# Performance work log

Hardware: AMD Instinct MI355X
Metric: run time of the kernel (lower is better)

## Reference

```python
import jax, jax.numpy as jnp
import numpy as np

N_NODES = 20000
N_EDGES = 320000
NFEAT = 50
ALPHA = 0.2  # leaky relu slope
EPS = 1e-16


def _gat_head(x, src, dst, W, a, concat):
    # x: (N, Fin), W: (Fin, Fout), a: (2*Fout,)
    N = x.shape[0]
    Wh = x @ W                      # (N, Fout)
    Fout = W.shape[1]
    # edge_h @ a == Wh[src] @ a[:Fout] + Wh[dst] @ a[Fout:]
    s_src = Wh @ a[:Fout]           # (N,)
    s_dst = Wh @ a[Fout:]           # (N,)
    e = jax.nn.leaky_relu(s_src[src] + s_dst[dst], negative_slope=ALPHA)  # (E,)
    # segment softmax over incoming edges of each target node
    e_max = jax.ops.segment_max(e, dst, num_segments=N)   # (N,)
    e_exp = jnp.exp(e - e_max[dst])                         # (E,)
    e_sum = jax.ops.segment_sum(e_exp, dst, num_segments=N)
    att = e_exp / (e_sum[dst] + EPS)                        # (E,)
    msg = Wh[src] * att[:, None]                            # (E, Fout)
    h = jax.ops.segment_sum(msg, dst, num_segments=N)       # (N, Fout)
    return jax.nn.elu(h) if concat else h


def _multi_head(x, src, dst, W, a, concat):
    # W: (H, Fin, Fout), a: (H, 2*Fout) -> (H, N, Fout)
    return jax.vmap(_gat_head, in_axes=(None, None, None, 0, 0, None))(x, src, dst, W, a, concat)


def setup_inputs() -> dict:
    key = jax.random.key(0)
    ks = jax.random.split(key, 8)
    x = jax.random.normal(ks[0], (N_NODES, NFEAT), dtype=jnp.float32)
    edge_index = jax.random.randint(ks[1], (2, N_EDGES), 0, N_NODES, dtype=jnp.int64)
    s = 0.1
    W1 = jax.random.normal(ks[2], (4, NFEAT, 256), dtype=jnp.float32) * s
    a1 = jax.random.normal(ks[3], (4, 512), dtype=jnp.float32) * s
    W2 = jax.random.normal(ks[4], (4, 1024, 256), dtype=jnp.float32) * s
    a2 = jax.random.normal(ks[5], (4, 512), dtype=jnp.float32) * s
    W3 = jax.random.normal(ks[6], (6, 1024, 121), dtype=jnp.float32) * s
    a3 = jax.random.normal(ks[7], (6, 242), dtype=jnp.float32) * s
    return {"x": x, "edge_index": edge_index, "W1": W1, "a1": a1, "W2": W2, "a2": a2, "W3": W3, "a3": a3}


def reference(x, edge_index, W1, a1, W2, a2, W3, a3):
    src, dst = edge_index[0], edge_index[1]
    N = x.shape[0]
    # layer 1: 4 heads, concat -> (N, 1024), then elu
    h1 = _multi_head(x, src, dst, W1, a1, True)      # (4, N, 256)
    x1 = jnp.transpose(h1, (1, 0, 2)).reshape(N, -1)  # concat along feature dim
    x1 = jax.nn.elu(x1)
    # layer 2: 4 heads, concat + skip connection, then elu
    h2 = _multi_head(x1, src, dst, W2, a2, True)
    x2 = jnp.transpose(h2, (1, 0, 2)).reshape(N, -1)
    x2 = jax.nn.elu(x2 + x1)
    # layer 3: 6 heads, no concat-elu, mean over heads
    h3 = _multi_head(x2, src, dst, W3, a3, False)     # (6, N, 121)
    x3 = jnp.mean(h3, axis=0)
    return jax.nn.sigmoid(x3)
```

## Files before the change

kernel.cpp:

```cpp
#include <hip/hip_runtime.h>
#include <cstdint>

#define N_NODES 20000
#define N_EDGES 320000
#define ALPHA 0.2f
#define GAT_EPS 1e-16f
#define MPAD 20096
#define RBLK 157
#define RHI 20
#define SCAN_BLKS 80
#define BT_ROWS 1152

typedef __attribute__((ext_vector_type(8))) _Float16 half8;
typedef __attribute__((ext_vector_type(4))) _Float16 half4t;
typedef __attribute__((ext_vector_type(16))) float f32x16;
typedef __attribute__((ext_vector_type(2))) float f32x2;

__device__ __forceinline__ float elu1(float x) { return x > 0.f ? x : __expf(x) - 1.f; }

__device__ __forceinline__ unsigned char f2fp8(float x) {
    return (unsigned char)(__builtin_amdgcn_cvt_pk_fp8_f32(x, 0.f, 0, false) & 0xff);
}

__device__ __forceinline__ void async16(const void* g, void* l) {
    __builtin_amdgcn_global_load_lds(
        (const __attribute__((address_space(1))) unsigned int*)g,
        (__attribute__((address_space(3))) unsigned int*)l, 16, 0, 0);
}

__device__ __forceinline__ float rdlanef(float v, int j) {
    return __int_as_float(__builtin_amdgcn_readlane(__float_as_int(v), j));
}

__global__ void hist_kernel(const int* __restrict__ dst, int* __restrict__ counts, int E) {
    int e = blockIdx.x * blockDim.x + threadIdx.x;
    if (e < E) atomicAdd(&counts[dst[e]], 1);
}

__global__ void scan1_kernel(const int* __restrict__ counts, int* __restrict__ excl,
                             int* __restrict__ partial, int N) {
    __shared__ int sh[256];
    int t = threadIdx.x, b = blockIdx.x;
    int i = b * 256 + t;
    int v = (i < N) ? counts[i] : 0;
    sh[t] = v;
    __syncthreads();
    for (int d = 1; d < 256; d <<= 1) {
        int x = (t >= d) ? sh[t - d] : 0;
        __syncthreads();
        sh[t] += x;
        __syncthreads();
    }
    if (i < N) excl[i] = sh[t] - v;
    if (t == 255) partial[b] = sh[255];
}

__global__ void scan2_kernel(int* __restrict__ partial) {
    __shared__ int sh[128];
    int t = threadIdx.x;
    int v = (t < SCAN_BLKS) ? partial[t] : 0;
    sh[t] = v;
    __syncthreads();
    for (int d = 1; d < 128; d <<= 1) {
        int x = (t >= d) ? sh[t - d] : 0;
        __syncthreads();
        sh[t] += x;
        __syncthreads();
    }
    if (t < SCAN_BLKS) partial[t] = sh[t] - v;
}

__global__ void scan3_kernel(const int* __restrict__ excl, const int* __restrict__ partial,
                             int* __restrict__ rowptr, int* __restrict__ cursor, int N, int E) {
    int t = threadIdx.x, b = blockIdx.x;
    int i = b * 256 + t;
    if (i < N) {
        int v = excl[i] + partial[b];
        rowptr[i] = v;
        cursor[i] = v;
    }
    if (i == 0) rowptr[N] = E;
}

__global__ void scatter_kernel(const int* __restrict__ src, const int* __restrict__ dst,
                               int* __restrict__ cursor, int* __restrict__ esrc, int E) {
    int e = blockIdx.x * blockDim.x + threadIdx.x;
    if (e < E) {
        int p = atomicAdd(&cursor[dst[e]], 1);
        esrc[p] = src[e];
    }
}

__global__ void pack_x16(const float* __restrict__ x, _Float16* __restrict__ A) {
    int idx = blockIdx.x * 256 + threadIdx.x;
    int r = idx >> 6, c = idx & 63;
    float v = (r < N_NODES && c < 50) ? x[r * 50 + c] : 0.f;
    A[idx] = (_Float16)v;
}

__global__ void pack_bt1(const float* __restrict__ W, _Float16* __restrict__ Bt) {
    int idx = blockIdx.x * 256 + threadIdx.x;
    int c = idx >> 6, k = idx & 63;
    int h = c >> 8, f = c & 255;
    float v = (k < 50) ? W[((size_t)h * 50 + k) * 256 + f] : 0.f;
    Bt[idx] = (_Float16)v;
}

__global__ void pack_bt16(const float* __restrict__ W, _Float16* __restrict__ Bt,
                          int F, int Fpad, int Ctot) {
    int c = blockIdx.y;
    int k = blockIdx.x * blockDim.x + threadIdx.x;
    float v = 0.f;
    if (c < Ctot) {
        int h = c / Fpad, f = c - h * Fpad;
        if (f < F) v = W[(size_t)h * 1024 * F + (size_t)k * F + f];
    }
    Bt[(size_t)c * 1024 + k] = (_Float16)v;
}

__global__ __launch_bounds__(64) void wtilde_kernel(const float* __restrict__ W,
                                                    const float* __restrict__ a,
                                                    _Float16* __restrict__ BT, int Kreal,
                                                    int Kdim, int F, int H, int Nfeat) {
    int k = blockIdx.x, j = blockIdx.y;
    if (j >= 2 * H) return;
    int lane = threadIdx.x;
    int h = j < H ? j : j - H;
    int ao = j < H ? 0 : F;
    float s = 0.f;
    if (k < Kreal) {
        const float* wp = W + ((size_t)h * Kreal + k) * F;
        const float* ap = a + (size_t)h * 2 * F + ao;
        for (int f = lane; f < F; f += 64) s += wp[f] * ap[f];
    }
#pragma unroll
    for (int off = 32; off; off >>= 1) s += __shfl_down(s, off);
    if (lane == 0) BT[(size_t)(Nfeat + j) * Kdim + k] = (_Float16)s;
}

__global__ __launch_bounds__(256) void gemm_f16(const _Float16* __restrict__ A,
                                                const _Float16* __restrict__ BT,
                                                unsigned char* __restrict__ C8,
                                                float* __restrict__ SPRE,
                                                int M, int Nfeat, int ld, int Kdim, int Cblk,
                                                int ldA, int mode) {
    int id = blockIdx.x;
    int xm = id & 7, q = id >> 3;
    int cb = q % Cblk, rh = q / Cblk;
    int rb = rh * 8 + xm;
    if (rb >= RBLK) return;
    __shared__ __align__(16) _Float16 sA[128 * 64];
    __shared__ __align__(16) _Float16 sB[128 * 64];
    int t = threadIdx.x;
    int row0 = rb * 128, col0 = cb * 128;
    int lane = t & 63, wave = t >> 6;
    int wm = wave >> 1, wn = wave & 1;
    int l31 = lane & 31;
    int lhi = lane >> 5;

    int koff = (mode == 1) ? ((cb >> 1) * 64) : 0;
    const _Float16* gA = A + (size_t)row0 * ldA + koff;
    const _Float16* gB = BT + (size_t)col0 * Kdim;

    int sR[4], sgl[4];
#pragma unroll
    for (int i = 0; i < 4; i++) {
        int m = i * 256 + t;
        sR[i] = m >> 3;
        sgl[i] = (m & 7) ^ (sR[i] & 7);
    }

    f32x16 acc[2][2] = {};

    for (int k0 = 0; k0 < Kdim; k0 += 64) {
        __syncthreads();
#pragma unroll
        for (int i = 0; i < 4; i++) {
            const _Float16* pa = gA + (size_t)sR[i] * ldA + k0 + sgl[i] * 8;
            const _Float16* pb = gB + (size_t)sR[i] * Kdim + k0 + sgl[i] * 8;
            async16(pa, sA + (i * 256 + t) * 8);
            async16(pb, sB + (i * 256 + t) * 8);
        }
        __syncthreads();
#pragma unroll
        for (int kk = 0; kk < 4; kk++) {
            int g = kk * 2 + lhi;
            half8 af[2], bf[2];
#pragma unroll
            for (int mt = 0; mt < 2; mt++) {
                int R = wm * 64 + mt * 32 + l31;
                int gp = g ^ (R & 7);
                af[mt] = *(const half8*)(sA + R * 64 + gp * 8);
            }
#pragma unroll
            for (int nt = 0; nt < 2; nt++) {
                int R = wn * 64 + nt * 32 + l31;
                int gp = g ^ (R & 7);
                bf[nt] = *(const half8*)(sB + R * 64 + gp * 8);
            }
#pragma unroll
            for (int mt = 0; mt < 2; mt++)
#pragma unroll
                for (int nt = 0; nt < 2; nt++)
                    acc[mt][nt] = __builtin_amdgcn_mfma_f32_32x32x16_f16(af[mt], bf[nt], acc[mt][nt], 0, 0, 0);
        }
    }

    int cb32 = col0 + wn * 64 + l31;
    int rb32 = row0 + wm * 64 + 4 * lhi;
    if (mode == 1) {
        _Float16* C16 = (_Float16*)C8;
#pragma unroll
        for (int mt = 0; mt < 2; mt++)
#pragma unroll
            for (int nt = 0; nt < 2; nt++) {
                int gc = cb32 + nt * 32;
                if (gc < Nfeat) {
#pragma unroll
                    for (int r = 0; r < 16; r++) {
                        int gr = rb32 + mt * 32 + (r & 3) + 8 * (r >> 2);
                        if (gr < M) C16[(size_t)gr * ld + gc] = (_Float16)elu1(elu1(acc[mt][nt][r]));
                    }
                }
            }
        return;
    }
#pragma unroll
    for (int mt = 0; mt < 2; mt++)
#pragma unroll
        for (int nt = 0; nt < 2; nt++) {
            int gc = cb32 + nt * 32;
            if (gc < Nfeat) {
#pragma unroll
                for (int r = 0; r < 16; r++) {
                    int gr = rb32 + mt * 32 + (r & 3) + 8 * (r >> 2);
                    if (gr < M) C8[(size_t)gr * ld + gc] = f2fp8(acc[mt][nt][r]);
                }
            } else if (gc < Nfeat + 12) {
                int j = gc - Nfeat;
#pragma unroll
                for (int r = 0; r < 16; r++) {
                    int gr = rb32 + mt * 32 + (r & 3) + 8 * (r >> 2);
                    if (gr < M) SPRE[(size_t)j * N_NODES + gr] = acc[mt][nt][r];
                }
            }
        }
}

__global__ __launch_bounds__(256) void aggx1_kernel(const int* __restrict__ rowptr,
                                                    const int* __restrict__ esrc,
                                                    const float* __restrict__ SPRE,
                                                    const _Float16* __restrict__ A1,
                                                    _Float16* __restrict__ XB, int N) {
    int n = blockIdx.x;
    int h = threadIdx.x >> 6;
    int lane = threadIdx.x & 63;
    int start = rowptr[n], end = rowptr[n + 1];
    int cnt = end - start;
    const float* ss = SPRE + (size_t)h * N;
    float sd = SPRE[(size_t)(4 + h) * N + n];
    const unsigned char* Wb = (const unsigned char*)A1 + 2 * lane;
    float acc = 0.f;

    if (cnt <= 64) {
        int e = start + lane;
        bool act = e < end;
        int idx = act ? esrc[e] : 0;
        int voff = idx << 7;

        unsigned short wA[8], wB[8], wC[8], wD[8];
        auto ISSUE = [&](unsigned short (&buf)[8], int base) {
#pragma unroll
            for (int u = 0; u < 8; u++) {
                int off = __builtin_amdgcn_readlane(voff, base + u);
                buf[u] = *(const unsigned short*)(Wb + (unsigned)off);
            }
        };
        ISSUE(wA, 0);
        if (cnt > 8)  ISSUE(wB, 8);
        if (cnt > 16) ISSUE(wC, 16);
        if (cnt > 24) ISSUE(wD, 24);

        float sc = -1e30f;
        if (act) {
            sc = ss[idx] + sd;
            sc = sc > 0.f ? sc : ALPHA * sc;
        }
        float m = sc;
#pragma unroll
        for (int off = 1; off < 64; off <<= 1) m = fmaxf(m, __shfl_xor(m, off));
        float ptil = act ? __expf(sc - m) : 0.f;
        float s = ptil;
#pragma unroll
        for (int off = 1; off < 64; off <<= 1) s += __shfl_xor(s, off);
        float p = ptil * (1.f / (s + GAT_EPS));

        auto CONSUME = [&](unsigned short (&buf)[8], int base) {
#pragma unroll
            for (int u = 0; u < 8; u++) {
                float pj = rdlanef(p, base + u);
                acc += pj * (float)(*(const _Float16*)&buf[u]);
            }
        };
        CONSUME(wA, 0);
        if (cnt > 8)  { if (cnt > 32) ISSUE(wA, 32); CONSUME(wB, 8); }
        if (cnt > 16) { if (cnt > 40) ISSUE(wB, 40); CONSUME(wC, 16); }
        if (cnt > 24) { if (cnt > 48) ISSUE(wC, 48); CONSUME(wD, 24); }
        if (cnt > 32) { if (cnt > 56) ISSUE(wD, 56); CONSUME(wA, 32); }
        if (cnt > 40) CONSUME(wB, 40);
        if (cnt > 48) CONSUME(wC, 48);
        if (cnt > 56) CONSUME(wD, 56);
    } else {
        float m = -1e30f, s = 0.f;
        int sidx = 0; float ssc = -1e30f;
        for (int e0 = start; e0 < end; e0 += 64) {
            int e = e0 + lane;
            bool act = e < end;
            int idx = act ? esrc[e] : 0;
            float sc = -1e30f;
            if (act) {
                sc = ss[idx] + sd;
                sc = sc > 0.f ? sc : ALPHA * sc;
            }
            sidx = idx; ssc = sc;
            float mn = fmaxf(m, sc);
            s = s * __expf(m - mn) + (act ? __expf(sc - mn) : 0.f);
            m = mn;
        }
        float lm = m;
#pragma unroll
        for (int off = 1; off < 64; off <<= 1) m = fmaxf(m, __shfl_xor(m, off));
        float ptil = s * __expf(lm - m);
        s = ptil;
#pragma unroll
        for (int off = 1; off < 64; off <<= 1) s += __shfl_xor(s, off);
        float inv = 1.f / (s + GAT_EPS);

        int lastStart = start + (((end - start - 1) >> 6) << 6);
        for (int e0 = start; e0 < end; e0 += 64) {
            int e = e0 + lane;
            bool act = e < end;
            int idx; float p;
            if (e0 == lastStart) {
                idx = sidx;
                p = act ? __expf(ssc - m) * inv : 0.f;
            } else {
                idx = act ? esrc[e] : 0;
                float sc = -1e30f;
                if (act) {
                    sc = ss[idx] + sd;
                    sc = sc > 0.f ? sc : ALPHA * sc;
                }
                p = act ? __expf(sc - m) * inv : 0.f;
            }
            int cn = end - e0; if (cn > 64) cn = 64;
            for (int j = 0; j < cn; j++) {
                int ij = __builtin_amdgcn_readlane(idx, j);
                float pj = rdlanef(p, j);
                unsigned short w = *(const unsigned short*)(Wb + ((size_t)(unsigned)ij << 7));
                acc += pj * (float)(*(const _Float16*)&w);
            }
        }
    }

    XB[(size_t)n * 256 + h * 64 + lane] = (_Float16)acc;
}

__global__ __launch_bounds__(256) void attagg256_kernel(const int* __restrict__ rowptr,
                                                        const int* __restrict__ esrc,
                                                        const float* __restrict__ SPRE,
                                                        const unsigned char* __restrict__ WH8,
                                                        _Float16* __restrict__ X16,
                                                        int use_skip, int N) {
    int n = blockIdx.x;
    int h = threadIdx.x >> 6;
    int lane = threadIdx.x & 63;
    int start = rowptr[n], end = rowptr[n + 1];
    int cnt = end - start;
    const float* ss = SPRE + (size_t)h * N;
    float sd = SPRE[(size_t)(4 + h) * N + n];
    const unsigned char* Wb = WH8 + h * 256 + lane * 4;
    float a0 = 0.f, a1 = 0.f, a2 = 0.f, a3 = 0.f;

    if (cnt <= 64) {
        int e = start + lane;
        bool act = e < end;
        int idx = act ? esrc[e] : 0;

        unsigned int wA[8], wB[8], wC[8], wD[8];
        auto ISSUE = [&](unsigned int (&buf)[8], int base) {
#pragma unroll
            for (int u = 0; u < 8; u++) {
                int ij = __builtin_amdgcn_readlane(idx, base + u);
                buf[u] = *(const unsigned int*)(Wb + ((size_t)(unsigned)ij << 10));
            }
        };
        ISSUE(wA, 0);
        if (cnt > 8)  ISSUE(wB, 8);
        if (cnt > 16) ISSUE(wC, 16);
        if (cnt > 24) ISSUE(wD, 24);

        float sc = -1e30f;
        if (act) {
            sc = ss[idx] + sd;
            sc = sc > 0.f ? sc : ALPHA * sc;
        }
        float m = sc;
#pragma unroll
        for (int off = 1; off < 64; off <<= 1) m = fmaxf(m, __shfl_xor(m, off));
        float ptil = act ? __expf(sc - m) : 0.f;
        float s = ptil;
#pragma unroll
        for (int off = 1; off < 64; off <<= 1) s += __shfl_xor(s, off);
        float p = ptil * (1.f / (s + GAT_EPS));

        auto CONSUME = [&](unsigned int (&buf)[8], int base) {
#pragma unroll
            for (int u = 0; u < 8; u++) {
                float pj = rdlanef(p, base + u);
                f32x2 lo = __builtin_amdgcn_cvt_pk_f32_fp8((int)buf[u], false);
                f32x2 hi = __builtin_amdgcn_cvt_pk_f32_fp8((int)buf[u], true);
                a0 += pj * lo.x; a1 += pj * lo.y; a2 += pj * hi.x; a3 += pj * hi.y;
            }
        };
        CONSUME(wA, 0);
        if (cnt > 8)  { if (cnt > 32) ISSUE(wA, 32); CONSUME(wB, 8); }
        if (cnt > 16) { if (cnt > 40) ISSUE(wB, 40); CONSUME(wC, 16); }
        if (cnt > 24) { if (cnt > 48) ISSUE(wC, 48); CONSUME(wD, 24); }
        if (cnt > 32) { if (cnt > 56) ISSUE(wD, 56); CONSUME(wA, 32); }
        if (cnt > 40) CONSUME(wB, 40);
        if (cnt > 48) CONSUME(wC, 48);
        if (cnt > 56) CONSUME(wD, 56);
    } else {
        float m = -1e30f, s = 0.f;
        int sidx = 0; float ssc = -1e30f;
        for (int e0 = start; e0 < end; e0 += 64) {
            int e = e0 + lane;
            bool act = e < end;
            int idx = act ? esrc[e] : 0;
            float sc = -1e30f;
            if (act) {
                sc = ss[idx] + sd;
                sc = sc > 0.f ? sc : ALPHA * sc;
            }
            sidx = idx; ssc = sc;
            float mn = fmaxf(m, sc);
            s = s * __expf(m - mn) + (act ? __expf(sc - mn) : 0.f);
            m = mn;
        }
        float lm = m;
#pragma unroll
        for (int off = 1; off < 64; off <<= 1) m = fmaxf(m, __shfl_xor(m, off));
        float ptil = s * __expf(lm - m);
        s = ptil;
#pragma unroll
        for (int off = 1; off < 64; off <<= 1) s += __shfl_xor(s, off);
        float inv = 1.f / (s + GAT_EPS);

        int lastStart = start + (((end - start - 1) >> 6) << 6);
        for (int e0 = start; e0 < end; e0 += 64) {
            int e = e0 + lane;
            bool act = e < end;
            int idx; float p;
            if (e0 == lastStart) {
                idx = sidx;
                p = act ? __expf(ssc - m) * inv : 0.f;
            } else {
                idx = act ? esrc[e] : 0;
                float sc = -1e30f;
                if (act) {
                    sc = ss[idx] + sd;
                    sc = sc > 0.f ? sc : ALPHA * sc;
                }
                p = act ? __expf(sc - m) * inv : 0.f;
            }
            int cn = end - e0; if (cn > 64) cn = 64;
            for (int j = 0; j < cn; j++) {
                int ij = __builtin_amdgcn_readlane(idx, j);
                float pj = rdlanef(p, j);
                unsigned int w = *(const unsigned int*)(Wb + (size_t)ij * 1024);
                f32x2 lo = __builtin_amdgcn_cvt_pk_f32_fp8((int)w, false);
                f32x2 hi = __builtin_amdgcn_cvt_pk_f32_fp8((int)w, true);
                a0 += pj * lo.x; a1 += pj * lo.y; a2 += pj * hi.x; a3 += pj * hi.y;
            }
        }
    }

    size_t o = (size_t)n * 1024 + h * 256 + lane * 4;
    float v0, v1, v2, v3;
    if (use_skip) {
        half4t sk = *(const half4t*)(X16 + o);
        v0 = elu1(elu1(a0) + (float)sk.x);
        v1 = elu1(elu1(a1) + (float)sk.y);
        v2 = elu1(elu1(a2) + (float)sk.z);
        v3 = elu1(elu1(a3) + (float)sk.w);
    } else {
        v0 = elu1(elu1(a0)); v1 = elu1(elu1(a1));
        v2 = elu1(elu1(a2)); v3 = elu1(elu1(a3));
    }
    half4t r;
    r.x = (_Float16)v0; r.y = (_Float16)v1; r.z = (_Float16)v2; r.w = (_Float16)v3;
    *(half4t*)(X16 + o) = r;
}

__global__ __launch_bounds__(384) void attagg726_kernel(const int* __restrict__ rowptr,
                                                        const int* __restrict__ esrc,
                                                        const float* __restrict__ SPRE,
                                                        const unsigned char* __restrict__ WH8,
                                                        float* __restrict__ out, int N) {
    __shared__ float part[6][124];
    int n = blockIdx.x;
    int t = threadIdx.x;
    int h = t >> 6;
    int lane = t & 63;
    int start = rowptr[n], end = rowptr[n + 1];
    int cnt = end - start;
    const float* ss = SPRE + (size_t)h * N;
    float sd = SPRE[(size_t)(6 + h) * N + n];
    const unsigned char* Wb = WH8 + h * 124 + 2 * lane;
    float a0 = 0.f, a1 = 0.f;

    if (cnt <= 64) {
        int e = start + lane;
        bool act = e < end;
        int idx = act ? esrc[e] : 0;

        unsigned short wA[8], wB[8], wC[8], wD[8];
        auto ISSUE = [&](unsigned short (&buf)[8], int base) {
#pragma unroll
            for (int u = 0; u < 8; u++) {
                int ij = __builtin_amdgcn_readlane(idx, base + u);
                buf[u] = *(const unsigned short*)(Wb + (size_t)(unsigned)ij * 768u);
            }
        };
        ISSUE(wA, 0);
        if (cnt > 8)  ISSUE(wB, 8);
        if (cnt > 16) ISSUE(wC, 16);
        if (cnt > 24) ISSUE(wD, 24);

        float sc = -1e30f;
        if (act) {
            sc = ss[idx] + sd;
            sc = sc > 0.f ? sc : ALPHA * sc;
        }
        float m = sc;
#pragma unroll
        for (int off = 1; off < 64; off <<= 1) m = fmaxf(m, __shfl_xor(m, off));
        float ptil = act ? __expf(sc - m) : 0.f;
        float s = ptil;
#pragma unroll
        for (int off = 1; off < 64; off <<= 1) s += __shfl_xor(s, off);
        float p = ptil * (1.f / (s + GAT_EPS));

        auto CONSUME = [&](unsigned short (&buf)[8], int base) {
#pragma unroll
            for (int u = 0; u < 8; u++) {
                float pj = rdlanef(p, base + u);
                f32x2 f = __builtin_amdgcn_cvt_pk_f32_fp8((int)buf[u], false);
                a0 += pj * f.x; a1 += pj * f.y;
            }
        };
        CONSUME(wA, 0);
        if (cnt > 8)  { if (cnt > 32) ISSUE(wA, 32); CONSUME(wB, 8); }
        if (cnt > 16) { if (cnt > 40) ISSUE(wB, 40); CONSUME(wC, 16); }
        if (cnt > 24) { if (cnt > 48) ISSUE(wC, 48); CONSUME(wD, 24); }
        if (cnt > 32) { if (cnt > 56) ISSUE(wD, 56); CONSUME(wA, 32); }
        if (cnt > 40) CONSUME(wB, 40);
        if (cnt > 48) CONSUME(wC, 48);
        if (cnt > 56) CONSUME(wD, 56);
    } else {
        float m = -1e30f, s = 0.f;
        int sidx = 0; float ssc = -1e30f;
        for (int e0 = start; e0 < end; e0 += 64) {
            int e = e0 + lane;
            bool act = e < end;
            int idx = act ? esrc[e] : 0;
            float sc = -1e30f;
            if (act) {
                sc = ss[idx] + sd;
                sc = sc > 0.f ? sc : ALPHA * sc;
            }
            sidx = idx; ssc = sc;
            float mn = fmaxf(m, sc);
            s = s * __expf(m - mn) + (act ? __expf(sc - mn) : 0.f);
            m = mn;
        }
        float lm = m;
#pragma unroll
        for (int off = 1; off < 64; off <<= 1) m = fmaxf(m, __shfl_xor(m, off));
        float ptil = s * __expf(lm - m);
        s = ptil;
#pragma unroll
        for (int off = 1; off < 64; off <<= 1) s += __shfl_xor(s, off);
        float inv = 1.f / (s + GAT_EPS);

        int lastStart = start + (((end - start - 1) >> 6) << 6);
        for (int e0 = start; e0 < end; e0 += 64) {
            int e = e0 + lane;
            bool act = e < end;
            int idx; float p;
            if (e0 == lastStart) {
                idx = sidx;
                p = act ? __expf(ssc - m) * inv : 0.f;
            } else {
                idx = act ? esrc[e] : 0;
                float sc = -1e30f;
                if (act) {
                    sc = ss[idx] + sd;
                    sc = sc > 0.f ? sc : ALPHA * sc;
                }
                p = act ? __expf(sc - m) * inv : 0.f;
            }
            int cn = end - e0; if (cn > 64) cn = 64;
            for (int j = 0; j < cn; j++) {
                int ij = __builtin_amdgcn_readlane(idx, j);
                float pj = rdlanef(p, j);
                unsigned short w = *(const unsigned short*)(Wb + (size_t)ij * 768);
                f32x2 f = __builtin_amdgcn_cvt_pk_f32_fp8((int)w, false);
                a0 += pj * f.x; a1 += pj * f.y;
            }
        }
    }

    if (lane < 62) {
        part[h][2 * lane]     = a0;
        part[h][2 * lane + 1] = a1;
    }
    __syncthreads();
    if (t < 121) {
        float tot = (part[0][t] + part[1][t] + part[2][t] +
                     part[3][t] + part[4][t] + part[5][t]) * (1.f / 6.f);
        out[(size_t)n * 121 + t] = 1.f / (1.f + __expf(-tot));
    }
}

extern "C" void kernel_launch(void* const* d_in, const int* in_sizes, int n_in,
                              void* d_out, int out_size, void* d_ws, size_t ws_size,
                              hipStream_t stream) {
    const float* x  = (const float*)d_in[0];
    const int*   ei = (const int*)d_in[1];
    const float* W1 = (const float*)d_in[2];
    const float* a1 = (const float*)d_in[3];
    const float* W2 = (const float*)d_in[4];
    const float* a2 = (const float*)d_in[5];
    const float* W3 = (const float*)d_in[6];
    const float* a3 = (const float*)d_in[7];
    float* out = (float*)d_out;
    const int N = N_NODES, E = N_EDGES;
    const int* src = ei;
    const int* dst = ei + E;

    char* ws = (char*)d_ws;
    size_t off = 0;
    auto alloc = [&](size_t b) { size_t o = off; off += (b + 255) & ~(size_t)255; return o; };
    _Float16* X16  = (_Float16*)(ws + alloc((size_t)MPAD * 1024 * 2));
    unsigned char* WH8 = (unsigned char*)(ws + alloc((size_t)MPAD * 1024));
    _Float16* BT16 = (_Float16*)(ws + alloc((size_t)BT_ROWS * 1024 * 2));
    _Float16* A1   = (_Float16*)(ws + alloc((size_t)MPAD * 64 * 2));
    _Float16* BT1  = (_Float16*)(ws + alloc((size_t)BT_ROWS * 64 * 2));
    _Float16* XB   = (_Float16*)(ws + alloc((size_t)MPAD * 256 * 2));
    _Float16* BTS  = (_Float16*)(ws + alloc((size_t)128 * 64 * 2));
    float* SPRE   = (float*)(ws + alloc((size_t)12 * N * 4));
    int*   rowptr = (int*)(ws + alloc((size_t)(N + 1) * 4));
    int*   cursor = (int*)(ws + alloc((size_t)N * 4));
    int*   counts = (int*)(ws + alloc((size_t)N * 4));
    int*   excl   = (int*)(ws + alloc((size_t)N * 4));
    int*   partial= (int*)(ws + alloc((size_t)SCAN_BLKS * 4));
    int*   esrc   = (int*)(ws + alloc((size_t)E * 4));

    hipMemsetAsync(counts, 0, (size_t)N * 4, stream);
    hist_kernel<<<(E + 255) / 256, 256, 0, stream>>>(dst, counts, E);
    scan1_kernel<<<SCAN_BLKS, 256, 0, stream>>>(counts, excl, partial, N);
    scan2_kernel<<<1, 128, 0, stream>>>(partial);
    scan3_kernel<<<SCAN_BLKS, 256, 0, stream>>>(excl, partial, rowptr, cursor, N, E);
    scatter_kernel<<<(E + 255) / 256, 256, 0, stream>>>(src, dst, cursor, esrc, E);
    hipMemsetAsync(X16 + (size_t)N * 1024, 0, (size_t)(MPAD - N) * 1024 * 2, stream);
    hipMemsetAsync(XB + (size_t)N * 256, 0, (size_t)(MPAD - N) * 256 * 2, stream);

    pack_x16<<<MPAD * 64 / 256, 256, 0, stream>>>(x, A1);
    pack_bt1<<<1024 * 64 / 256, 256, 0, stream>>>(W1, BT1);
    wtilde_kernel<<<dim3(64, 8), 64, 0, stream>>>(W1, a1, BTS, 50, 64, 256, 4, 0);
    gemm_f16<<<8 * RHI * 1, 256, 0, stream>>>(A1, BTS, WH8, SPRE, N, 0, 1024, 64, 1, 64, 0);
    aggx1_kernel<<<N, 256, 0, stream>>>(rowptr, esrc, SPRE, A1, XB, N);
    gemm_f16<<<8 * RHI * 8, 256, 0, stream>>>(XB, BT1, (unsigned char*)X16, SPRE, N, 1024, 1024, 64, 8, 256, 1);

    pack_bt16<<<dim3(4, 1024), 256, 0, stream>>>(W2, BT16, 256, 256, 1024);
    wtilde_kernel<<<dim3(1024, 8), 64, 0, stream>>>(W2, a2, BT16, 1024, 1024, 256, 4, 1024);
    gemm_f16<<<8 * RHI * 9, 256, 0, stream>>>(X16, BT16, WH8, SPRE, N, 1024, 1024, 1024, 9, 1024, 0);
    attagg256_kernel<<<N, 256, 0, stream>>>(rowptr, esrc, SPRE, WH8, X16, 1, N);

    pack_bt16<<<dim3(4, 744), 256, 0, stream>>>(W3, BT16, 121, 124, 744);
    wtilde_kernel<<<dim3(1024, 12), 64, 0, stream>>>(W3, a3, BT16, 1024, 1024, 121, 6, 744);
    gemm_f16<<<8 * RHI * 6, 256, 0, stream>>>(X16, BT16, WH8, SPRE, N, 744, 768, 1024, 6, 1024, 0);
    attagg726_kernel<<<N, 384, 0, stream>>>(rowptr, esrc, SPRE, WH8, out, N);
}
```

Baseline: 434.2 us.

## Split aggregation across edges per wave with 16-byte row loads and LDS reduction

The layer-2 and layer-3 aggregation kernels now give each wave a strided subset of edges instead of one head. Each lane loads 16 contiguous fp8 bytes of a full neighbor row and accumulates with packed FMA, and per-wave partials are summed through shared memory. To keep rows aligned, the layer-3 projection output is padded to 128 columns per head with a 1024-byte stride. The aim is wider, fully coalesced gathers with more loads in flight, at the cost of extra LDS traffic, two block barriers and a slightly larger layer-3 GEMM.

```diff
diff --git a/kernel.cpp b/kernel.cpp
--- a/kernel.cpp
+++ b/kernel.cpp
@@ -30,6 +30,17 @@
 
 __device__ __forceinline__ float rdlanef(float v, int j) {
     return __int_as_float(__builtin_amdgcn_readlane(__float_as_int(v), j));
+}
+
+__device__ __forceinline__ f32x2 pkfma(f32x2 a, f32x2 b, f32x2 c) {
+    f32x2 d;
+    asm("v_pk_fma_f32 %0, %1, %2, %3" : "=v"(d) : "v"(a), "v"(b), "v"(c));
+    return d;
+}
+
+template <bool HI>
+__device__ __forceinline__ f32x2 cvt8(unsigned int u) {
+    return __builtin_amdgcn_cvt_pk_f32_fp8((int)u, HI);
 }
 
 __global__ void hist_kernel(const int* __restrict__ dst, int* __restrict__ counts, int E) {
@@ -372,33 +383,33 @@
                                                         const unsigned char* __restrict__ WH8,
                                                         _Float16* __restrict__ X16,
                                                         int use_skip, int N) {
+    __shared__ float Pp[4][66];
+    __shared__ float part[4][1152];
     int n = blockIdx.x;
-    int h = threadIdx.x >> 6;
-    int lane = threadIdx.x & 63;
+    int t = threadIdx.x;
+    int wv = t >> 6;
+    int lane = t & 63;
     int start = rowptr[n], end = rowptr[n + 1];
     int cnt = end - start;
-    const float* ss = SPRE + (size_t)h * N;
-    float sd = SPRE[(size_t)(4 + h) * N + n];
-    const unsigned char* Wb = WH8 + h * 256 + lane * 4;
-    float a0 = 0.f, a1 = 0.f, a2 = 0.f, a3 = 0.f;
+    const float* ss = SPRE + (size_t)wv * N;
+    float sd = SPRE[(size_t)(4 + wv) * N + n];
 
     if (cnt <= 64) {
         int e = start + lane;
         bool act = e < end;
         int idx = act ? esrc[e] : 0;
 
-        unsigned int wA[8], wB[8], wC[8], wD[8];
-        auto ISSUE = [&](unsigned int (&buf)[8], int base) {
-#pragma unroll
-            for (int u = 0; u < 8; u++) {
-                int ij = __builtin_amdgcn_readlane(idx, base + u);
-                buf[u] = *(const unsigned int*)(Wb + ((size_t)(unsigned)ij << 10));
-            }
-        };
-        ISSUE(wA, 0);
-        if (cnt > 8)  ISSUE(wB, 8);
-        if (cnt > 16) ISSUE(wC, 16);
-        if (cnt > 24) ISSUE(wD, 24);
+        const unsigned char* Wp = WH8 + lane * 16;
+        uint4 w = {}, wnext = {};
+        bool has0 = wv < cnt, has1 = wv + 4 < cnt;
+        if (has0) {
+            int i0 = __builtin_amdgcn_readlane(idx, wv);
+            w = *(const uint4*)(Wp + ((size_t)(unsigned)i0 << 10));
+        }
+        if (has1) {
+            int i1 = __builtin_amdgcn_readlane(idx, wv + 4);
+            wnext = *(const uint4*)(Wp + ((size_t)(unsigned)i1 << 10));
+        }
 
         float sc = -1e30f;
         if (act) {
@@ -413,25 +424,42 @@
 #pragma unroll
         for (int off = 1; off < 64; off <<= 1) s += __shfl_xor(s, off);
         float p = ptil * (1.f / (s + GAT_EPS));
-
-        auto CONSUME = [&](unsigned int (&buf)[8], int base) {
-#pragma unroll
-            for (int u = 0; u < 8; u++) {
-                float pj = rdlanef(p, base + u);
-                f32x2 lo = __builtin_amdgcn_cvt_pk_f32_fp8((int)buf[u], false);
-                f32x2 hi = __builtin_amdgcn_cvt_pk_f32_fp8((int)buf[u], true);
-                a0 += pj * lo.x; a1 += pj * lo.y; a2 += pj * hi.x; a3 += pj * hi.y;
-            }
-        };
-        CONSUME(wA, 0);
-        if (cnt > 8)  { if (cnt > 32) ISSUE(wA, 32); CONSUME(wB, 8); }
-        if (cnt > 16) { if (cnt > 40) ISSUE(wB, 40); CONSUME(wC, 16); }
-        if (cnt > 24) { if (cnt > 48) ISSUE(wC, 48); CONSUME(wD, 24); }
-        if (cnt > 32) { if (cnt > 56) ISSUE(wD, 56); CONSUME(wA, 32); }
-        if (cnt > 40) CONSUME(wB, 40);
-        if (cnt > 48) CONSUME(wC, 48);
-        if (cnt > 56) CONSUME(wD, 56);
+        Pp[wv][lane] = p;
+        __syncthreads();
+
+        f32x2 acc[8] = {};
+        int hf = lane >> 4;
+        if (has0) {
+            int j = wv;
+            for (;;) {
+                uint4 w3 = w;
+                bool have3 = j + 8 < cnt;
+                if (have3) {
+                    int i3 = __builtin_amdgcn_readlane(idx, j + 8);
+                    w3 = *(const uint4*)(Wp + ((size_t)(unsigned)i3 << 10));
+                }
+                float pj = Pp[hf][j];
+                f32x2 pv; pv.x = pj; pv.y = pj;
+                acc[0] = pkfma(cvt8<false>(w.x), pv, acc[0]);
+                acc[1] = pkfma(cvt8<true>(w.x),  pv, acc[1]);
+                acc[2] = pkfma(cvt8<false>(w.y), pv, acc[2]);
+                acc[3] = pkfma(cvt8<true>(w.y),  pv, acc[3]);
+                acc[4] = pkfma(cvt8<false>(w.z), pv, acc[4]);
+                acc[5] = pkfma(cvt8<true>(w.z),  pv, acc[5]);
+                acc[6] = pkfma(cvt8<false>(w.w), pv, acc[6]);
+                acc[7] = pkfma(cvt8<true>(w.w),  pv, acc[7]);
+                j += 4;
+                if (j >= cnt) break;
+                w = wnext; wnext = w3;
+            }
+        }
+#pragma unroll
+        for (int k2 = 0; k2 < 8; k2++)
+            *(f32x2*)&part[wv][lane * 18 + 2 * k2] = acc[k2];
     } else {
+        for (int i = lane; i < 1152; i += 64) part[wv][i] = 0.f;
+        const unsigned char* Wb = WH8 + wv * 256 + lane * 4;
+        float a0 = 0.f, a1 = 0.f, a2 = 0.f, a3 = 0.f;
         float m = -1e30f, s = 0.f;
         int sidx = 0; float ssc = -1e30f;
         for (int e0 = start; e0 < end; e0 += 64) {
@@ -478,15 +506,28 @@
             for (int j = 0; j < cn; j++) {
                 int ij = __builtin_amdgcn_readlane(idx, j);
                 float pj = rdlanef(p, j);
-                unsigned int w = *(const unsigned int*)(Wb + (size_t)ij * 1024);
-                f32x2 lo = __builtin_amdgcn_cvt_pk_f32_fp8((int)w, false);
-                f32x2 hi = __builtin_amdgcn_cvt_pk_f32_fp8((int)w, true);
+                unsigned int ww = *(const unsigned int*)(Wb + (size_t)ij * 1024);
+                f32x2 lo = __builtin_amdgcn_cvt_pk_f32_fp8((int)ww, false);
+                f32x2 hi = __builtin_amdgcn_cvt_pk_f32_fp8((int)ww, true);
                 a0 += pj * lo.x; a1 += pj * lo.y; a2 += pj * hi.x; a3 += pj * hi.y;
             }
         }
-    }
-
-    size_t o = (size_t)n * 1024 + h * 256 + lane * 4;
+        int cb = wv * 256 + lane * 4;
+        int off0 = (cb >> 4) * 18 + (cb & 15);
+        part[wv][off0]     = a0;
+        part[wv][off0 + 1] = a1;
+        part[wv][off0 + 2] = a2;
+        part[wv][off0 + 3] = a3;
+    }
+    __syncthreads();
+
+    int off = (t >> 2) * 18 + 4 * (t & 3);
+    float a0 = part[0][off]     + part[1][off]     + part[2][off]     + part[3][off];
+    float a1 = part[0][off + 1] + part[1][off + 1] + part[2][off + 1] + part[3][off + 1];
+    float a2 = part[0][off + 2] + part[1][off + 2] + part[2][off + 2] + part[3][off + 2];
+    float a3 = part[0][off + 3] + part[1][off + 3] + part[2][off + 3] + part[3][off + 3];
+
+    size_t o = (size_t)n * 1024 + t * 4;
     float v0, v1, v2, v3;
     if (use_skip) {
         half4t sk = *(const half4t*)(X16 + o);
@@ -508,35 +549,36 @@
                                                         const float* __restrict__ SPRE,
                                                         const unsigned char* __restrict__ WH8,
                                                         float* __restrict__ out, int N) {
-    __shared__ float part[6][124];
+    __shared__ float Pp[6][66];
+    __shared__ float part[6][864];
+    __shared__ float red[768];
     int n = blockIdx.x;
     int t = threadIdx.x;
-    int h = t >> 6;
+    int wv = t >> 6;
     int lane = t & 63;
     int start = rowptr[n], end = rowptr[n + 1];
     int cnt = end - start;
-    const float* ss = SPRE + (size_t)h * N;
-    float sd = SPRE[(size_t)(6 + h) * N + n];
-    const unsigned char* Wb = WH8 + h * 124 + 2 * lane;
-    float a0 = 0.f, a1 = 0.f;
+    const float* ss = SPRE + (size_t)wv * N;
+    float sd = SPRE[(size_t)(6 + wv) * N + n];
 
     if (cnt <= 64) {
         int e = start + lane;
         bool act = e < end;
         int idx = act ? esrc[e] : 0;
 
-        unsigned short wA[8], wB[8], wC[8], wD[8];
-        auto ISSUE = [&](unsigned short (&buf)[8], int base) {
-#pragma unroll
-            for (int u = 0; u < 8; u++) {
-                int ij = __builtin_amdgcn_readlane(idx, base + u);
-                buf[u] = *(const unsigned short*)(Wb + (size_t)(unsigned)ij * 768u);
-            }
-        };
-        ISSUE(wA, 0);
-        if (cnt > 8)  ISSUE(wB, 8);
-        if (cnt > 16) ISSUE(wC, 16);
-        if (cnt > 24) ISSUE(wD, 24);
+        const unsigned char* Wp = WH8 + lane * 16;
+        uint4 w = {}, wnext = {};
+        bool has0 = wv < cnt, has1 = wv + 6 < cnt;
+        if (lane < 48) {
+            if (has0) {
+                int i0 = __builtin_amdgcn_readlane(idx, wv);
+                w = *(const uint4*)(Wp + ((size_t)(unsigned)i0 << 10));
+            }
+            if (has1) {
+                int i1 = __builtin_amdgcn_readlane(idx, wv + 6);
+                wnext = *(const uint4*)(Wp + ((size_t)(unsigned)i1 << 10));
+            }
+        }
 
         float sc = -1e30f;
         if (act) {
@@ -551,24 +593,44 @@
 #pragma unroll
         for (int off = 1; off < 64; off <<= 1) s += __shfl_xor(s, off);
         float p = ptil * (1.f / (s + GAT_EPS));
-
-        auto CONSUME = [&](unsigned short (&buf)[8], int base) {
-#pragma unroll
-            for (int u = 0; u < 8; u++) {
-                float pj = rdlanef(p, base + u);
-                f32x2 f = __builtin_amdgcn_cvt_pk_f32_fp8((int)buf[u], false);
-                a0 += pj * f.x; a1 += pj * f.y;
-            }
-        };
-        CONSUME(wA, 0);
-        if (cnt > 8)  { if (cnt > 32) ISSUE(wA, 32); CONSUME(wB, 8); }
-        if (cnt > 16) { if (cnt > 40) ISSUE(wB, 40); CONSUME(wC, 16); }
-        if (cnt > 24) { if (cnt > 48) ISSUE(wC, 48); CONSUME(wD, 24); }
-        if (cnt > 32) { if (cnt > 56) ISSUE(wD, 56); CONSUME(wA, 32); }
-        if (cnt > 40) CONSUME(wB, 40);
-        if (cnt > 48) CONSUME(wC, 48);
-        if (cnt > 56) CONSUME(wD, 56);
+        Pp[wv][lane] = p;
+        __syncthreads();
+
+        f32x2 acc[8] = {};
+        if (lane < 48 && has0) {
+            int hf = lane >> 3;
+            int j = wv;
+            for (;;) {
+                uint4 w3 = w;
+                bool have3 = j + 12 < cnt;
+                if (have3) {
+                    int i3 = __builtin_amdgcn_readlane(idx, j + 12);
+                    w3 = *(const uint4*)(Wp + ((size_t)(unsigned)i3 << 10));
+                }
+                float pj = Pp[hf][j];
+                f32x2 pv; pv.x = pj; pv.y = pj;
+                acc[0] = pkfma(cvt8<false>(w.x), pv, acc[0]);
+                acc[1] = pkfma(cvt8<true>(w.x),  pv, acc[1]);
+                acc[2] = pkfma(cvt8<false>(w.y), pv, acc[2]);
+                acc[3] = pkfma(cvt8<true>(w.y),  pv, acc[3]);
+                acc[4] = pkfma(cvt8<false>(w.z), pv, acc[4]);
+                acc[5] = pkfma(cvt8<true>(w.z),  pv, acc[5]);
+                acc[6] = pkfma(cvt8<false>(w.w), pv, acc[6]);
+                acc[7] = pkfma(cvt8<true>(w.w),  pv, acc[7]);
+                j += 6;
+                if (j >= cnt) break;
+                w = wnext; wnext = w3;
+            }
+        }
+        if (lane < 48) {
+#pragma unroll
+            for (int k2 = 0; k2 < 8; k2++)
+                *(f32x2*)&part[wv][lane * 18 + 2 * k2] = acc[k2];
+        }
     } else {
+        for (int i = lane; i < 864; i += 64) part[wv][i] = 0.f;
+        const unsigned char* Wb = WH8 + wv * 128 + 2 * lane;
+        float a0 = 0.f, a1 = 0.f;
         float m = -1e30f, s = 0.f;
         int sidx = 0; float ssc = -1e30f;
         for (int e0 = start; e0 < end; e0 += 64) {
@@ -615,21 +677,27 @@
             for (int j = 0; j < cn; j++) {
                 int ij = __builtin_amdgcn_readlane(idx, j);
                 float pj = rdlanef(p, j);
-                unsigned short w = *(const unsigned short*)(Wb + (size_t)ij * 768);
-                f32x2 f = __builtin_amdgcn_cvt_pk_f32_fp8((int)w, false);
+                unsigned short ww = *(const unsigned short*)(Wb + ((size_t)(unsigned)ij << 10));
+                f32x2 f = __builtin_amdgcn_cvt_pk_f32_fp8((int)ww, false);
                 a0 += pj * f.x; a1 += pj * f.y;
             }
         }
-    }
-
-    if (lane < 62) {
-        part[h][2 * lane]     = a0;
-        part[h][2 * lane + 1] = a1;
+        int c0 = wv * 128 + 2 * lane;
+        part[wv][(c0 >> 4) * 18 + (c0 & 15)] = a0;
+        int c1 = c0 + 1;
+        part[wv][(c1 >> 4) * 18 + (c1 & 15)] = a1;
+    }
+    __syncthreads();
+
+    for (int c = t; c < 768; c += 384) {
+        int off = (c >> 4) * 18 + (c & 15);
+        red[c] = part[0][off] + part[1][off] + part[2][off] +
+                 part[3][off] + part[4][off] + part[5][off];
     }
     __syncthreads();
     if (t < 121) {
-        float tot = (part[0][t] + part[1][t] + part[2][t] +
-                     part[3][t] + part[4][t] + part[5][t]) * (1.f / 6.f);
+        float tot = (red[t] + red[128 + t] + red[256 + t] +
+                     red[384 + t] + red[512 + t] + red[640 + t]) * (1.f / 6.f);
         out[(size_t)n * 121 + t] = 1.f / (1.f + __expf(-tot));
     }
 }
@@ -689,8 +757,8 @@
     gemm_f16<<<8 * RHI * 9, 256, 0, stream>>>(X16, BT16, WH8, SPRE, N, 1024, 1024, 1024, 9, 1024, 0);
     attagg256_kernel<<<N, 256, 0, stream>>>(rowptr, esrc, SPRE, WH8, X16, 1, N);
 
-    pack_bt16<<<dim3(4, 744), 256, 0, stream>>>(W3, BT16, 121, 124, 744);
-    wtilde_kernel<<<dim3(1024, 12), 64, 0, stream>>>(W3, a3, BT16, 1024, 1024, 121, 6, 744);
-    gemm_f16<<<8 * RHI * 6, 256, 0, stream>>>(X16, BT16, WH8, SPRE, N, 744, 768, 1024, 6, 1024, 0);
+    pack_bt16<<<dim3(4, 768), 256, 0, stream>>>(W3, BT16, 121, 128, 768);
+    wtilde_kernel<<<dim3(1024, 12), 64, 0, stream>>>(W3, a3, BT16, 1024, 1024, 121, 6, 768);
+    gemm_f16<<<8 * RHI * 7, 256, 0, stream>>>(X16, BT16, WH8, SPRE, N, 768, 1024, 1024, 7, 1024, 0);
     attagg726_kernel<<<N, 384, 0, stream>>>(rowptr, esrc, SPRE, WH8, out, N);
 }
```

After: 438.6 us. About the same (+1.0%).

## Split layer-2 attention into softmax precompute and column-chunked aggregation kernel

Applied to the files above, without the earlier changes.

The fused layer-2 attention+aggregation kernel is split in two. A new att_kernel computes normalized edge attention per head into a buffer. A new agg256c_kernel gives each block 4 nodes times one 128-column chunk, so a wave gathers 2 fp8 bytes per lane instead of 4. Column chunks are ordered so that blocks sharing a chunk run close together, which should improve cache locality of the neighbour-row gathers. The cost is an extra launch, an attention buffer write and read, and more gather instructions in total.

```diff
diff --git a/kernel.cpp b/kernel.cpp
--- a/kernel.cpp
+++ b/kernel.cpp
@@ -30,6 +30,11 @@
 
 __device__ __forceinline__ float rdlanef(float v, int j) {
     return __int_as_float(__builtin_amdgcn_readlane(__float_as_int(v), j));
+}
+
+template <bool HI>
+__device__ __forceinline__ f32x2 cvt8(unsigned int u) {
+    return __builtin_amdgcn_cvt_pk_f32_fp8((int)u, HI);
 }
 
 __global__ void hist_kernel(const int* __restrict__ dst, int* __restrict__ counts, int E) {
@@ -366,33 +371,101 @@
     XB[(size_t)n * 256 + h * 64 + lane] = (_Float16)acc;
 }
 
-__global__ __launch_bounds__(256) void attagg256_kernel(const int* __restrict__ rowptr,
-                                                        const int* __restrict__ esrc,
-                                                        const float* __restrict__ SPRE,
-                                                        const unsigned char* __restrict__ WH8,
-                                                        _Float16* __restrict__ X16,
-                                                        int use_skip, int N) {
+__global__ void att_kernel(const int* __restrict__ rowptr, const int* __restrict__ esrc,
+                           const float* __restrict__ SPRE, float* __restrict__ ATT,
+                           int N, int H) {
     int n = blockIdx.x;
     int h = threadIdx.x >> 6;
     int lane = threadIdx.x & 63;
+    if (h >= H) return;
     int start = rowptr[n], end = rowptr[n + 1];
     int cnt = end - start;
     const float* ss = SPRE + (size_t)h * N;
-    float sd = SPRE[(size_t)(4 + h) * N + n];
-    const unsigned char* Wb = WH8 + h * 256 + lane * 4;
-    float a0 = 0.f, a1 = 0.f, a2 = 0.f, a3 = 0.f;
+    float sd = SPRE[(size_t)(H + h) * N + n];
+    float* ap = ATT + (size_t)h * N_EDGES;
 
     if (cnt <= 64) {
         int e = start + lane;
         bool act = e < end;
         int idx = act ? esrc[e] : 0;
-
-        unsigned int wA[8], wB[8], wC[8], wD[8];
-        auto ISSUE = [&](unsigned int (&buf)[8], int base) {
+        float sc = -1e30f;
+        if (act) {
+            sc = ss[idx] + sd;
+            sc = sc > 0.f ? sc : ALPHA * sc;
+        }
+        float m = sc;
+#pragma unroll
+        for (int off = 1; off < 64; off <<= 1) m = fmaxf(m, __shfl_xor(m, off));
+        float ptil = act ? __expf(sc - m) : 0.f;
+        float s = ptil;
+#pragma unroll
+        for (int off = 1; off < 64; off <<= 1) s += __shfl_xor(s, off);
+        if (act) ap[e] = ptil * (1.f / (s + GAT_EPS));
+    } else {
+        float m = -1e30f, s = 0.f;
+        for (int e0 = start; e0 < end; e0 += 64) {
+            int e = e0 + lane;
+            bool act = e < end;
+            int idx = act ? esrc[e] : 0;
+            float sc = -1e30f;
+            if (act) {
+                sc = ss[idx] + sd;
+                sc = sc > 0.f ? sc : ALPHA * sc;
+            }
+            float mn = fmaxf(m, sc);
+            s = s * __expf(m - mn) + (act ? __expf(sc - mn) : 0.f);
+            m = mn;
+        }
+        float lm = m;
+#pragma unroll
+        for (int off = 1; off < 64; off <<= 1) m = fmaxf(m, __shfl_xor(m, off));
+        float ptil = s * __expf(lm - m);
+        s = ptil;
+#pragma unroll
+        for (int off = 1; off < 64; off <<= 1) s += __shfl_xor(s, off);
+        float inv = 1.f / (s + GAT_EPS);
+        for (int e0 = start; e0 < end; e0 += 64) {
+            int e = e0 + lane;
+            if (e < end) {
+                int idx = esrc[e];
+                float sc = ss[idx] + sd;
+                sc = sc > 0.f ? sc : ALPHA * sc;
+                ap[e] = __expf(sc - m) * inv;
+            }
+        }
+    }
+}
+
+__global__ __launch_bounds__(256) void agg256c_kernel(const int* __restrict__ rowptr,
+                                                      const int* __restrict__ esrc,
+                                                      const float* __restrict__ ATT,
+                                                      const unsigned char* __restrict__ WH8,
+                                                      _Float16* __restrict__ X16, int N) {
+    int id = blockIdx.x;
+    int c = id & 7;
+    int g = id >> 3;
+    int wv = threadIdx.x >> 6;
+    int lane = threadIdx.x & 63;
+    int n = g * 4 + wv;
+    if (n >= N) return;
+    int start = rowptr[n], end = rowptr[n + 1];
+    int cnt = end - start;
+    const float* ap = ATT + (size_t)(c >> 1) * N_EDGES;
+    const unsigned char* Wb = WH8 + c * 128 + lane * 2;
+    float a0 = 0.f, a1 = 0.f;
+
+    if (cnt <= 64) {
+        int e = start + lane;
+        bool act = e < end;
+        int idx = act ? esrc[e] : 0;
+        float p = act ? ap[e] : 0.f;
+
+        unsigned short wA[8], wB[8], wC[8], wD[8];
+        auto ISSUE = [&](unsigned short (&buf)[8], int base) {
 #pragma unroll
             for (int u = 0; u < 8; u++) {
                 int ij = __builtin_amdgcn_readlane(idx, base + u);
-                buf[u] = *(const unsigned int*)(Wb + ((size_t)(unsigned)ij << 10));
+                buf[u] = *(const unsigned short*)(Wb + ((size_t)(unsigned)ij << 10));
             }
         };
         ISSUE(wA, 0);
@@ -400,6 +473,82 @@
         if (cnt > 16) ISSUE(wC, 16);
         if (cnt > 24) ISSUE(wD, 24);
 
+        auto CONSUME = [&](unsigned short (&buf)[8], int base) {
+#pragma unroll
+            for (int u = 0; u < 8; u++) {
+                float pj = rdlanef(p, base + u);
+                f32x2 f = cvt8<false>(buf[u]);
+                a0 += pj * f.x; a1 += pj * f.y;
+            }
+        };
+        CONSUME(wA, 0);
+        if (cnt > 8)  { if (cnt > 32) ISSUE(wA, 32); CONSUME(wB, 8); }
+        if (cnt > 16) { if (cnt > 40) ISSUE(wB, 40); CONSUME(wC, 16); }
+        if (cnt > 24) { if (cnt > 48) ISSUE(wC, 48); CONSUME(wD, 24); }
+        if (cnt > 32) { if (cnt > 56) ISSUE(wD, 56); CONSUME(wA, 32); }
+        if (cnt > 40) CONSUME(wB, 40);
+        if (cnt > 48) CONSUME(wC, 48);
+        if (cnt > 56) CONSUME(wD, 56);
+    } else {
+        for (int e0 = start; e0 < end; e0 += 64) {
+            int e = e0 + lane;
+            bool act = e < end;
+            int idx = act ? esrc[e] : 0;
+            float p = act ? ap[e] : 0.f;
+            int cn = end - e0; if (cn > 64) cn = 64;
+            for (int j = 0; j < cn; j++) {
+                int ij = __builtin_amdgcn_readlane(idx, j);
+                float pj = rdlanef(p, j);
+                unsigned short w = *(const unsigned short*)(Wb + ((size_t)(unsigned)ij << 10));
+                f32x2 f = cvt8<false>(w);
+                a0 += pj * f.x; a1 += pj * f.y;
+            }
+        }
+    }
+
+    size_t o = (size_t)n * 1024 + c * 128 + lane * 2;
+    union { unsigned int u; _Float16 hh[2]; } sk, wr;
+    sk.u = *(const unsigned int*)(X16 + o);
+    wr.hh[0] = (_Float16)elu1(elu1(a0) + (float)sk.hh[0]);
+    wr.hh[1] = (_Float16)elu1(elu1(a1) + (float)sk.hh[1]);
+    *(unsigned int*)(X16 + o) = wr.u;
+}
+
+__global__ __launch_bounds__(384) void attagg726_kernel(const int* __restrict__ rowptr,
+                                                        const int* __restrict__ esrc,
+                                                        const float* __restrict__ SPRE,
+                                                        const unsigned char* __restrict__ WH8,
+                                                        float* __restrict__ out, int N) {
+    __shared__ float part[6][124];
+    int n = blockIdx.x;
+    int t = threadIdx.x;
+    int h = t >> 6;
+    int lane = t & 63;
+    int start = rowptr[n], end = rowptr[n + 1];
+    int cnt = end - start;
+    const float* ss = SPRE + (size_t)h * N;
+    float sd = SPRE[(size_t)(6 + h) * N + n];
+    const unsigned char* Wb = WH8 + h * 124 + 2 * lane;
+    float a0 = 0.f, a1 = 0.f;
+
+    if (cnt <= 64) {
+        int e = start + lane;
+        bool act = e < end;
+        int idx = act ? esrc[e] : 0;
+
+        unsigned short wA[8], wB[8], wC[8], wD[8];
+        auto ISSUE = [&](unsigned short (&buf)[8], int base) {
+#pragma unroll
+            for (int u = 0; u < 8; u++) {
+                int ij = __builtin_amdgcn_readlane(idx, base + u);
+                buf[u] = *(const unsigned short*)(Wb + (size_t)(unsigned)ij * 768u);
+            }
+        };
+        ISSUE(wA, 0);
+        if (cnt > 8)  ISSUE(wB, 8);
+        if (cnt > 16) ISSUE(wC, 16);
+        if (cnt > 24) ISSUE(wD, 24);
+
         float sc = -1e30f;
         if (act) {
             sc = ss[idx] + sd;
@@ -414,13 +563,12 @@
         for (int off = 1; off < 64; off <<= 1) s += __shfl_xor(s, off);
         float p = ptil * (1.f / (s + GAT_EPS));
 
-        auto CONSUME = [&](unsigned int (&buf)[8], int base) {
+        auto CONSUME = [&](unsigned short (&buf)[8], int base) {
 #pragma unroll
             for (int u = 0; u < 8; u++) {
                 float pj = rdlanef(p, base + u);
-                f32x2 lo = __builtin_amdgcn_cvt_pk_f32_fp8((int)buf[u], false);
-                f32x2 hi = __builtin_amdgcn_cvt_pk_f32_fp8((int)buf[u], true);
-                a0 += pj * lo.x; a1 += pj * lo.y; a2 += pj * hi.x; a3 += pj * hi.y;
+                f32x2 f = cvt8<false>(buf[u]);
+                a0 += pj * f.x; a1 += pj * f.y;
             }
         };
         CONSUME(wA, 0);
@@ -475,149 +623,14 @@
                 p = act ? __expf(sc - m) * inv : 0.f;
             }
             int cn = end - e0; if (cn > 64) cn = 64;
-            for (int j = 0; j < cn; j++) {
-                int ij = __builtin_amdgcn_readlane(idx, j);
-                float pj = rdlanef(p, j);
-                unsigned int w = *(const unsigned int*)(Wb + (size_t)ij * 1024);
-                f32x2 lo = __builtin_amdgcn_cvt_pk_f32_fp8((int)w, false);
-                f32x2 hi = __builtin_amdgcn_cvt_pk_f32_fp8((int)w, true);
-                a0 += pj * lo.x; a1 += pj * lo.y; a2 += pj * hi.x; a3 += pj * hi.y;
-            }
-        }
-    }
-
-    size_t o = (size_t)n * 1024 + h * 256 + lane * 4;
-    float v0, v1, v2, v3;
-    if (use_skip) {
-        half4t sk = *(const half4t*)(X16 + o);
-        v0 = elu1(elu1(a0) + (float)sk.x);
-        v1 = elu1(elu1(a1) + (float)sk.y);
-        v2 = elu1(elu1(a2) + (float)sk.z);
-        v3 = elu1(elu1(a3) + (float)sk.w);
-    } else {
-        v0 = elu1(elu1(a0)); v1 = elu1(elu1(a1));
-        v2 = elu1(elu1(a2)); v3 = elu1(elu1(a3));
-    }
-    half4t r;
-    r.x = (_Float16)v0; r.y = (_Float16)v1; r.z = (_Float16)v2; r.w = (_Float16)v3;
-    *(half4t*)(X16 + o) = r;
-}
-
-__global__ __launch_bounds__(384) void attagg726_kernel(const int* __restrict__ rowptr,
-                                                        const int* __restrict__ esrc,
-                                                        const float* __restrict__ SPRE,
-                                                        const unsigned char* __restrict__ WH8,
-                                                        float* __restrict__ out, int N) {
-    __shared__ float part[6][124];
-    int n = blockIdx.x;
-    int t = threadIdx.x;
-    int h = t >> 6;
-    int lane = t & 63;
-    int start = rowptr[n], end = rowptr[n + 1];
-    int cnt = end - start;
-    const float* ss = SPRE + (size_t)h * N;
-    float sd = SPRE[(size_t)(6 + h) * N + n];
-    const unsigned char* Wb = WH8 + h * 124 + 2 * lane;
-    float a0 = 0.f, a1 = 0.f;
-
-    if (cnt <= 64) {
-        int e = start + lane;
-        bool act = e < end;
-        int idx = act ? esrc[e] : 0;
-
-        unsigned short wA[8], wB[8], wC[8], wD[8];
-        auto ISSUE = [&](unsigned short (&buf)[8], int base) {
-#pragma unroll
-            for (int u = 0; u < 8; u++) {
-                int ij = __builtin_amdgcn_readlane(idx, base + u);
-                buf[u] = *(const unsigned short*)(Wb + (size_t)(unsigned)ij * 768u);
-            }
-        };
-        ISSUE(wA, 0);
-        if (cnt > 8)  ISSUE(wB, 8);
-        if (cnt > 16) ISSUE(wC, 16);
-        if (cnt > 24) ISSUE(wD, 24);
-
-        float sc = -1e30f;
-        if (act) {
-            sc = ss[idx] + sd;
-            sc = sc > 0.f ? sc : ALPHA * sc;
-        }
-        float m = sc;
-#pragma unroll
-        for (int off = 1; off < 64; off <<= 1) m = fmaxf(m, __shfl_xor(m, off));
-        float ptil = act ? __expf(sc - m) : 0.f;
-        float s = ptil;
-#pragma unroll
-        for (int off = 1; off < 64; off <<= 1) s += __shfl_xor(s, off);
-        float p = ptil * (1.f / (s + GAT_EPS));
-
-        auto CONSUME = [&](unsigned short (&buf)[8], int base) {
-#pragma unroll
-            for (int u = 0; u < 8; u++) {
-                float pj = rdlanef(p, base + u);
-                f32x2 f = __builtin_amdgcn_cvt_pk_f32_fp8((int)buf[u], false);
-                a0 += pj * f.x; a1 += pj * f.y;
-            }
-        };
-        CONSUME(wA, 0);
-        if (cnt > 8)  { if (cnt > 32) ISSUE(wA, 32); CONSUME(wB, 8); }
-        if (cnt > 16) { if (cnt > 40) ISSUE(wB, 40); CONSUME(wC, 16); }
-        if (cnt > 24) { if (cnt > 48) ISSUE(wC, 48); CONSUME(wD, 24); }
-        if (cnt > 32) { if (cnt > 56) ISSUE(wD, 56); CONSUME(wA, 32); }
-        if (cnt > 40) CONSUME(wB, 40);
-        if (cnt > 48) CONSUME(wC, 48);
-        if (cnt > 56) CONSUME(wD, 56);
-    } else {
-        float m = -1e30f, s = 0.f;
-        int sidx = 0; float ssc = -1e30f;
-        for (int e0 = start; e0 < end; e0 += 64) {
-            int e = e0 + lane;
-            bool act = e < end;
-            int idx = act ? esrc[e] : 0;
-            float sc = -1e30f;
-            if (act) {
-                sc = ss[idx] + sd;
-                sc = sc > 0.f ? sc : ALPHA * sc;
-            }
-            sidx = idx; ssc = sc;
-            float mn = fmaxf(m, sc);
-            s = s * __expf(m - mn) + (act ? __expf(sc - mn) : 0.f);
-            m = mn;
-        }
-        float lm = m;
-#pragma unroll
-        for (int off = 1; off < 64; off <<= 1) m = fmaxf(m, __shfl_xor(m, off));
-        float ptil = s * __expf(lm - m);
-        s = ptil;
-#pragma unroll
-        for (int off = 1; off < 64; off <<= 1) s += __shfl_xor(s, off);
-        float inv = 1.f / (s + GAT_EPS);
-
-        int lastStart = start + (((end - start - 1) >> 6) << 6);
-        for (int e0 = start; e0 < end; e0 += 64) {
-            int e = e0 + lane;
-            bool act = e < end;
-            int idx; float p;
-            if (e0 == lastStart) {
-                idx = sidx;
-                p = act ? __expf(ssc - m) * inv : 0.f;
-            } else {
-                idx = act ? esrc[e] : 0;
-                float sc = -1e30f;
-                if (act) {
-                    sc = ss[idx] + sd;
-                    sc = sc > 0.f ? sc : ALPHA * sc;
+            if (lane < 62) {
+                for (int j = 0; j < cn; j++) {
+                    int ij = __builtin_amdgcn_readlane(idx, j);
+                    float pj = rdlanef(p, j);
+                    unsigned short w = *(const unsigned short*)(Wb + (size_t)ij * 768);
+                    f32x2 f = cvt8<false>(w);
+                    a0 += pj * f.x; a1 += pj * f.y;
                 }
-                p = act ? __expf(sc - m) * inv : 0.f;
-            }
-            int cn = end - e0; if (cn > 64) cn = 64;
-            for (int j = 0; j < cn; j++) {
-                int ij = __builtin_amdgcn_readlane(idx, j);
-                float pj = rdlanef(p, j);
-                unsigned short w = *(const unsigned short*)(Wb + (size_t)ij * 768);
-                f32x2 f = __builtin_amdgcn_cvt_pk_f32_fp8((int)w, false);
-                a0 += pj * f.x; a1 += pj * f.y;
             }
         }
     }
@@ -661,6 +674,7 @@
     _Float16* XB   = (_Float16*)(ws + alloc((size_t)MPAD * 256 * 2));
     _Float16* BTS  = (_Float16*)(ws + alloc((size_t)128 * 64 * 2));
     float* SPRE   = (float*)(ws + alloc((size_t)12 * N * 4));
+    float* ATT    = (float*)(ws + alloc((size_t)4 * E * 4));
     int*   rowptr = (int*)(ws + alloc((size_t)(N + 1) * 4));
     int*   cursor = (int*)(ws + alloc((size_t)N * 4));
     int*   counts = (int*)(ws + alloc((size_t)N * 4));
@@ -687,7 +701,8 @@
     pack_bt16<<<dim3(4, 1024), 256, 0, stream>>>(W2, BT16, 256, 256, 1024);
     wtilde_kernel<<<dim3(1024, 8), 64, 0, stream>>>(W2, a2, BT16, 1024, 1024, 256, 4, 1024);
     gemm_f16<<<8 * RHI * 9, 256, 0, stream>>>(X16, BT16, WH8, SPRE, N, 1024, 1024, 1024, 9, 1024, 0);
-    attagg256_kernel<<<N, 256, 0, stream>>>(rowptr, esrc, SPRE, WH8, X16, 1, N);
+    att_kernel<<<N, 256, 0, stream>>>(rowptr, esrc, SPRE, ATT, N, 4);
+    agg256c_kernel<<<(N / 4) * 8, 256, 0, stream>>>(rowptr, esrc, ATT, WH8, X16, N);
 
     pack_bt16<<<dim3(4, 744), 256, 0, stream>>>(W3, BT16, 121, 124, 744);
     wtilde_kernel<<<dim3(1024, 12), 64, 0, stream>>>(W3, a3, BT16, 1024, 1024, 121, 6, 744);
```

Result: slower. 456.5 us (+5.1%).
